# Performance work log

Hardware: AMD Instinct MI355X
Metric: run time of the kernel (lower is better)

## Reference

```python
import jax, jax.numpy as jnp
import numpy as np

T, B, DIN, H, AA, L = 1024, 32, 256, 256, 21, 2


def setup_inputs() -> dict:
    key = jax.random.key(0)
    ks = jax.random.split(key, 8)
    scale = 0.05

    def rn(i, shape):
        return jax.random.normal(ks[i], shape, dtype=jnp.float32) * scale

    return {
        "x": jax.random.normal(ks[0], (B, T, DIN), dtype=jnp.float32),
        "hidden": jnp.zeros((2 * L, B, H), jnp.float32),  # accepted but unused, as in torch forward
        # layer 0: input DIN -> per-direction 4 chunks of H; layer 1: input 2H
        "w_l0": rn(1, (DIN, 2, 4, H)),
        "wc_l0": rn(2, (2, 2, H)),            # [dir, (v_f, v_r), H]
        "b_l0": jnp.zeros((2, 2, H), jnp.float32),  # [dir, (b_f, b_r), H]
        "w_l1": rn(3, (2 * H, 2, 4, H)),
        "wc_l1": rn(4, (2, 2, H)),
        "b_l1": jnp.zeros((2, 2, H), jnp.float32),
        "fc1_w": rn(5, (H, 2 * H)),
        "fc1_b": jnp.zeros((H,), jnp.float32),
        "lp_w": rn(6, (AA, H)),
        "lp_b": jnp.zeros((AA,), jnp.float32),
    }


def _sru_scan(u, vf, vr, bf, br):
    # u: (T, B, 4, H) with chunks [candidate, forget, reset, highway]
    def step(c, ut):
        f = jax.nn.sigmoid(ut[:, 1] + vf * c + bf)
        c2 = f * c + (1.0 - f) * ut[:, 0]
        r = jax.nn.sigmoid(ut[:, 2] + vr * c + br)
        h = r * c2 + (1.0 - r) * ut[:, 3]
        return c2, h

    c0 = jnp.zeros((u.shape[1], u.shape[-1]), u.dtype)
    _, hs = jax.lax.scan(step, c0, u)
    return hs  # (T, B, H)


def _sru_layer(x, w, wc, b):
    # x: (T, B, Din); w: (Din, 2, 4, H)
    U = jnp.einsum('tbd,dnkh->tbnkh', x, w)
    hf = _sru_scan(U[:, :, 0], wc[0, 0], wc[0, 1], b[0, 0], b[0, 1])
    hb = _sru_scan(U[::-1, :, 1], wc[1, 0], wc[1, 1], b[1, 0], b[1, 1])[::-1]
    return jnp.concatenate([hf, hb], axis=-1)  # (T, B, 2H)


def reference(x, hidden, w_l0, wc_l0, b_l0, w_l1, wc_l1, b_l1, fc1_w, fc1_b, lp_w, lp_b):
    h = jnp.transpose(x, (1, 0, 2))  # (T, B, DIN)
    h = _sru_layer(h, w_l0, wc_l0, b_l0)
    h = _sru_layer(h, w_l1, wc_l1, b_l1)
    h = jnp.transpose(h, (1, 0, 2))  # (B, T, 2H)
    h = h @ fc1_w.T + fc1_b
    logits = h @ lp_w.T + lp_b
    return jax.nn.log_softmax(logits, axis=-1)  # (B, T, AA)
```

## Files before the change

### kernel.cpp

```cpp
#include <hip/hip_runtime.h>
#include <hip/hip_bf16.h>

#define T_DIM 1024
#define B_DIM 32
#define DIN_DIM 256
#define H_DIM 256
#define AA_DIM 21
#define M_ROWS (B_DIM * T_DIM)

typedef __attribute__((ext_vector_type(8))) short bf16x8;
typedef __attribute__((ext_vector_type(4))) float f32x4;

typedef __attribute__((address_space(3))) void lds_void;
typedef const __attribute__((address_space(1))) void glb_void;

#define LOG2E_F 1.44269504088896340736f

__device__ __forceinline__ void gload_lds16(const void* g, void* l) {
    __builtin_amdgcn_global_load_lds((glb_void*)g, (lds_void*)l, 16, 0, 0);
}

__device__ __forceinline__ unsigned short f2bu(float f) {
    __hip_bfloat16 h = __float2bfloat16(f);
    unsigned short u;
    __builtin_memcpy(&u, &h, 2);
    return u;
}

#define CVT_V0 2097152
#define CVT_N1 524288
#define CVT_N2 1048576
#define CVT_V3 32768
#define CVT_N4 8192
#define CVT_TOT (CVT_V0 + CVT_N1 + CVT_N2 + CVT_V3 + CVT_N4)
__global__ __launch_bounds__(256) void cvt_all(
    const float* __restrict__ x,  const float* __restrict__ w0,
    const float* __restrict__ w1, const float* __restrict__ fcw,
    const float* __restrict__ lpw,
    __hip_bfloat16* __restrict__ xb,  __hip_bfloat16* __restrict__ w0t,
    __hip_bfloat16* __restrict__ w1t, __hip_bfloat16* __restrict__ fcwb,
    __hip_bfloat16* __restrict__ lpwb)
{
    int i = blockIdx.x * 256 + threadIdx.x;
    if (i < CVT_V0) {
        float4 v = ((const float4*)x)[i];
        ushort4 o = { f2bu(v.x), f2bu(v.y), f2bu(v.z), f2bu(v.w) };
        ((ushort4*)xb)[i] = o;
        return;
    }
    i -= CVT_V0;
    if (i < CVT_N1) {
        int kk = i >> 11, rem = i & 2047;
        int dir = rem >> 10, k = (rem >> 8) & 3, h = rem & 255;
        w0t[(long)(dir * 1024 + h * 4 + k) * 256 + kk] = __float2bfloat16(w0[i]);
        return;
    }
    i -= CVT_N1;
    if (i < CVT_N2) {
        int kk = i >> 11, rem = i & 2047;
        int dir = rem >> 10, k = (rem >> 8) & 3, h = rem & 255;
        w1t[(long)(dir * 1024 + h * 4 + k) * 512 + kk] = __float2bfloat16(w1[i]);
        return;
    }
    i -= CVT_N2;
    if (i < CVT_V3) {
        float4 v = ((const float4*)fcw)[i];
        ushort4 o = { f2bu(v.x), f2bu(v.y), f2bu(v.z), f2bu(v.w) };
        ((ushort4*)fcwb)[i] = o;
        return;
    }
    i -= CVT_V3;
    if (i < CVT_N4) {
        int n = i >> 8, k = i & 255;
        lpwb[i] = __float2bfloat16(n < AA_DIM ? lpw[n * 256 + k] : 0.0f);
    }
}

#define MFMA16(d, a, b) d = __builtin_amdgcn_mfma_f32_16x16x32_bf16(a, b, d, 0, 0, 0)

__device__ __forceinline__ void stage_tile256(
    const __hip_bfloat16* __restrict__ A,
    const __hip_bfloat16* __restrict__ Bt,
    char* buf, long m0, long n0, int K, int kb,
    int wave, int ldrow, int gkoff)
{
#pragma unroll
    for (int i = 0; i < 4; ++i) {
        const int cid = wave * 4 + i;
        const int rc  = cid >> 1;
        const int kh  = cid & 1;
        const long row = rc * 16 + ldrow;
        const int koff = kb + kh * 32 + gkoff;
        gload_lds16(A  + (m0 + row) * (long)K + koff,
                    buf + rc * 2048 + kh * 1024);
        gload_lds16(Bt + (n0 + row) * (long)K + koff,
                    buf + 32768 + rc * 2048 + kh * 1024);
    }
}

__global__ __launch_bounds__(512, 2) void gemm256_u2(
    const __hip_bfloat16* __restrict__ A,
    const __hip_bfloat16* __restrict__ Bt,
    __hip_bfloat16* __restrict__ C,
    int K, int nbShift)
{
    __shared__ __align__(16) char smb[131072];

    const int tid  = threadIdx.x;
    const int lane = tid & 63;
    const int wave = tid >> 6;
    const int wm   = wave >> 2;
    const int wn   = wave & 3;

    const int L  = blockIdx.x;
    const int s  = L >> 3;
    const int nb = s & ((1 << nbShift) - 1);
    const int mb = ((s >> nbShift) << 3) + (L & 7);
    const long n0 = (long)nb * 256;
    const long m0 = (long)mb * 256;

    const int ldrow = lane >> 2;
    const int ldq   = lane & 3;
    const int gq    = ldq ^ ((ldrow >> 1) & 3);
    const int gkoff = gq * 8;

    const int fr = lane & 15;
    const int kq = lane >> 4;
    const int sw = (kq ^ ((fr >> 1) & 3)) * 16;

    f32x4 acc[8][4] = {};
    const int NT = K >> 6;

    stage_tile256(A, Bt, smb,         m0, n0, K, 0,  wave, ldrow, gkoff);
    __builtin_amdgcn_sched_barrier(0);
    stage_tile256(A, Bt, smb + 65536, m0, n0, K, 64, wave, ldrow, gkoff);
    asm volatile("s_waitcnt vmcnt(8)" ::: "memory");
    __builtin_amdgcn_s_barrier();

    for (int kt = 0; kt < NT; ++kt) {
        char* rb = smb + (kt & 1) * 65536;
        const char* Ab = rb + (wm * 8) * 2048;
        const char* Bb = rb + 32768 + (wn * 4) * 2048;
        bf16x8 a0[4], a1[4], bv[4];

#pragma unroll
        for (int i = 0; i < 4; ++i) {
            a0[i] = *(const bf16x8*)(Ab + i * 2048 + fr * 64 + sw);
            bv[i] = *(const bf16x8*)(Bb + i * 2048 + fr * 64 + sw);
        }
        __builtin_amdgcn_s_barrier();
        __builtin_amdgcn_s_setprio(1);
#pragma unroll
        for (int i = 0; i < 4; ++i)
#pragma unroll
            for (int j = 0; j < 4; ++j)
                MFMA16(acc[i][j], a0[i], bv[j]);
        __builtin_amdgcn_s_setprio(0);
        __builtin_amdgcn_s_barrier();

#pragma unroll
        for (int i = 0; i < 4; ++i)
            a1[i] = *(const bf16x8*)(Ab + (4 + i) * 2048 + fr * 64 + sw);
        __builtin_amdgcn_s_barrier();
        __builtin_amdgcn_s_setprio(1);
#pragma unroll
        for (int i = 0; i < 4; ++i)
#pragma unroll
            for (int j = 0; j < 4; ++j)
                MFMA16(acc[4 + i][j], a1[i], bv[j]);
        __builtin_amdgcn_s_setprio(0);
        __builtin_amdgcn_s_barrier();

#pragma unroll
        for (int i = 0; i < 4; ++i) {
            a0[i] = *(const bf16x8*)(Ab + i * 2048 + 1024 + fr * 64 + sw);
            bv[i] = *(const bf16x8*)(Bb + i * 2048 + 1024 + fr * 64 + sw);
        }
        __builtin_amdgcn_s_barrier();
        __builtin_amdgcn_s_setprio(1);
#pragma unroll
        for (int i = 0; i < 4; ++i)
#pragma unroll
            for (int j = 0; j < 4; ++j)
                MFMA16(acc[i][j], a0[i], bv[j]);
        __builtin_amdgcn_s_setprio(0);
        __builtin_amdgcn_s_barrier();

#pragma unroll
        for (int i = 0; i < 4; ++i)
            a1[i] = *(const bf16x8*)(Ab + (4 + i) * 2048 + 1024 + fr * 64 + sw);
        __builtin_amdgcn_s_barrier();
        __builtin_amdgcn_s_setprio(1);
#pragma unroll
        for (int i = 0; i < 4; ++i)
#pragma unroll
            for (int j = 0; j < 4; ++j)
                MFMA16(acc[4 + i][j], a1[i], bv[j]);
        __builtin_amdgcn_s_setprio(0);
        __builtin_amdgcn_s_barrier();

        __builtin_amdgcn_sched_barrier(0);
        if (kt + 2 < NT) {
            stage_tile256(A, Bt, rb, m0, n0, K, (kt + 2) * 64,
                          wave, ldrow, gkoff);
            asm volatile("s_waitcnt vmcnt(8)" ::: "memory");
        } else if (kt + 1 < NT) {
            asm volatile("s_waitcnt vmcnt(0)" ::: "memory");
        }
        __builtin_amdgcn_s_barrier();
    }

    const int col_l = lane & 15;
    const int row_l = (lane >> 4) * 4;
    __hip_bfloat16* smC = (__hip_bfloat16*)smb;
    const int chunk = tid & 31;
    const int rbase = tid >> 5;
#pragma unroll
    for (int p = 0; p < 2; ++p) {
        __syncthreads();
        if (wm == p) {
#pragma unroll
            for (int i = 0; i < 8; ++i)
#pragma unroll
                for (int j = 0; j < 4; ++j)
#pragma unroll
                    for (int r = 0; r < 4; ++r)
                        smC[(i * 16 + row_l + r) * 264 + wn * 64 + j * 16 + col_l] =
                            __float2bfloat16(acc[i][j][r]);
        }
        __syncthreads();
#pragma unroll
        for (int it = 0; it < 8; ++it) {
            const int rr = it * 16 + rbase;
            bf16x8 v = *(const bf16x8*)(smC + rr * 264 + chunk * 8);
            const long gr  = m0 + p * 128 + rr;
            const long gc0 = n0 + chunk * 8;
            const int bI  = (int)(gr >> 10);
            const int t   = (int)(gr & 1023);
            const int dir = (int)(gc0 >> 10);
            const int hg  = ((int)gc0 >> 8) & 3;
            const int beta = bI * 8 + dir * 4 + hg;
            const long base = ((long)beta * 1024 + t) * 256 + ((int)gc0 & 255);
            *(bf16x8*)(C + base) = v;
        }
    }
}

#define SCAN_S 64
#define SCAN_NB (T_DIM / SCAN_S)
#define GRP 16

__device__ __forceinline__ float scan_step(
    uint2 u, float c, float nvf, float nvr, float nbf, float nbr,
    __hip_bfloat16* hq)
{
    float u0, u1, u2, u3;
    unsigned a0 = u.x << 16, a1 = u.x & 0xffff0000u;
    unsigned a2 = u.y << 16, a3 = u.y & 0xffff0000u;
    __builtin_memcpy(&u0, &a0, 4); __builtin_memcpy(&u1, &a1, 4);
    __builtin_memcpy(&u2, &a2, 4); __builtin_memcpy(&u3, &a3, 4);
    const float nf0 = __builtin_fmaf(-LOG2E_F, u1, nbf);
    const float nr0 = __builtin_fmaf(-LOG2E_F, u2, nbr);
    const float ef = __builtin_amdgcn_exp2f(__builtin_fmaf(nvf, c, nf0));
    const float er = __builtin_amdgcn_exp2f(__builtin_fmaf(nvr, c, nr0));
    const float f  = __builtin_amdgcn_rcpf(1.0f + ef);
    const float r  = __builtin_amdgcn_rcpf(1.0f + er);
    const float c2 = __builtin_fmaf(f, c - u0, u0);
    const float hv = __builtin_fmaf(r, c2 - u3, u3);
    *hq = __float2bfloat16(hv);
    return c2;
}

__global__ __launch_bounds__(256) void sru_scan(
    const __hip_bfloat16* __restrict__ U2,
    const float* __restrict__ wc,
    const float* __restrict__ bias,
    __hip_bfloat16* __restrict__ hout)
{
    __shared__ __align__(16) char lds[2 * SCAN_S * 512];
    const int tid  = threadIdx.x;
    const int wave = tid >> 6;
    const int lane = tid & 63;
    const int beta = blockIdx.x;
    const int b    = beta >> 3;
    const int dir  = (beta >> 2) & 1;
    const int hg   = beta & 3;
    const int h    = hg * 64 + lane;

    const char* gslice = (const char*)U2 + (size_t)beta * (1024 * 512);

    const float nvf = -LOG2E_F * wc[(dir * 2 + 0) * H_DIM + h];
    const float nvr = -LOG2E_F * wc[(dir * 2 + 1) * H_DIM + h];
    const float nbf = -LOG2E_F * bias[(dir * 2 + 0) * H_DIM + h];
    const float nbr = -LOG2E_F * bias[(dir * 2 + 1) * H_DIM + h];
    __hip_bfloat16* hp = hout + ((long)(b * 1024 + (dir ? 1023 : 0))) * 512 + dir * 256 + h;
    const long hstep = dir ? -512L : 512L;
    float c = 0.0f;

    const int plane = lane & 31;

    if (wave > 0) {
        for (int p = wave - 1; p < SCAN_S / 2; p += 3) {
            const int sl = 2 * p + (lane >> 5);
            const int t  = dir ? (1023 - sl) : sl;
            gload_lds16(gslice + (size_t)t * 512 + plane * 16, lds + p * 1024);
        }
    }
    __syncthreads();

    for (int bat = 0; bat < SCAN_NB; ++bat) {
        if (wave > 0) {
            if (bat + 1 < SCAN_NB) {
                char* halfN = lds + ((bat + 1) & 1) * (SCAN_S * 512);
                const int tb = (bat + 1) * SCAN_S;
                for (int p = wave - 1; p < SCAN_S / 2; p += 3) {
                    const int sl = tb + 2 * p + (lane >> 5);
                    const int t  = dir ? (1023 - sl) : sl;
                    gload_lds16(gslice + (size_t)t * 512 + plane * 16,
                                halfN + p * 1024);
                }
            }
        } else {
            const char* half = lds + (bat & 1) * (SCAN_S * 512);
            __hip_bfloat16* hq = hp + (long)(bat * SCAN_S) * hstep;
            uint2 qa[GRP], qb[GRP];
#pragma unroll
            for (int j = 0; j < GRP; ++j)
                qa[j] = *(const uint2*)(half + (0 * GRP + j) * 512 + (lane << 3));
#pragma unroll
            for (int j = 0; j < GRP; ++j)
                qb[j] = *(const uint2*)(half + (1 * GRP + j) * 512 + (lane << 3));
#pragma unroll
            for (int j = 0; j < GRP; ++j)
                c = scan_step(qa[j], c, nvf, nvr, nbf, nbr, hq + (long)j * hstep);
#pragma unroll
            for (int j = 0; j < GRP; ++j)
                qa[j] = *(const uint2*)(half + (2 * GRP + j) * 512 + (lane << 3));
#pragma unroll
            for (int j = 0; j < GRP; ++j)
                c = scan_step(qb[j], c, nvf, nvr, nbf, nbr, hq + (long)(GRP + j) * hstep);
#pragma unroll
            for (int j = 0; j < GRP; ++j)
                qb[j] = *(const uint2*)(half + (3 * GRP + j) * 512 + (lane << 3));
#pragma unroll
            for (int j = 0; j < GRP; ++j)
                c = scan_step(qa[j], c, nvf, nvr, nbf, nbr, hq + (long)(2 * GRP + j) * hstep);
#pragma unroll
            for (int j = 0; j < GRP; ++j)
                c = scan_step(qb[j], c, nvf, nvr, nbf, nbr, hq + (long)(3 * GRP + j) * hstep);
        }
        __syncthreads();
    }
}

#define FL_BUF 49152
#define FL_LP  98304
#define FL_SCR 115200
#define FL_TOT 133632

__global__ __launch_bounds__(512, 1) void fc_logits(
    const __hip_bfloat16* __restrict__ A,
    const __hip_bfloat16* __restrict__ Bw,
    const float* __restrict__ fcb,
    const __hip_bfloat16* __restrict__ lpwb,
    const float* __restrict__ lpb,
    float* __restrict__ out)
{
    __shared__ __align__(16) char lds[FL_TOT];
    const int tid  = threadIdx.x;
    const int lane = tid & 63;
    const int wave = tid >> 6;
    const int wm   = wave & 1;
    const int wn   = wave >> 1;
    const long m0  = (long)blockIdx.x * 128;

    const int ldrow = lane >> 2;
    const int ldq   = lane & 3;
    const int gq    = ldq ^ ((ldrow >> 1) & 3);
    const int gkoff = gq * 8;

    const int fr = lane & 15;
    const int kq = lane >> 4;
    const int sw = (kq ^ ((fr >> 1) & 3)) * 16;

    for (int idx = tid; idx < 1024; idx += 512) {
        const int rw = idx >> 5, sl = idx & 31;
        *(bf16x8*)(lds + FL_LP + rw * 528 + sl * 16) =
            *(const bf16x8*)(lpwb + rw * 256 + sl * 8);
    }
    __builtin_amdgcn_sched_barrier(0);

    f32x4 acc[4][4] = {};

#define STAGE_FL(BUF, KB)                                                   \
    do {                                                                    \
        _Pragma("unroll")                                                   \
        for (int i2 = 0; i2 < 6; ++i2) {                                    \
            const int sg = wave * 6 + i2;                        \
            if (sg < 16) {                              \
                const int rc = sg >> 1, kh = sg & 1;                        \
                gload_lds16(A + (m0 + rc * 16 + ldrow) * 512L +             \
                                (KB) + kh * 32 + gkoff,                     \
                            (BUF) + rc * 2048 + kh * 1024);                 \
            } else {                                   \
                const int t2 = sg - 16, rc = t2 >> 1, kh = t2 & 1;          \
                gload_lds16(Bw + (rc * 16 + ldrow) * 512L +                 \
                                 (KB) + kh * 32 + gkoff,                    \
                            (BUF) + 16384 + rc * 2048 + kh * 1024);         \
            }                                                               \
        }                                                                   \
    } while (0)

    STAGE_FL(lds, 0);

    for (int kt = 0; kt < 8; ++kt) {
        char* cur = lds + (kt & 1) * FL_BUF;
        char* nxt = lds + ((kt + 1) & 1) * FL_BUF;
        __builtin_amdgcn_sched_barrier(0);
        if (kt + 1 < 8) {
            STAGE_FL(nxt, (kt + 1) * 64);
            __builtin_amdgcn_sched_barrier(0);
            asm volatile("s_waitcnt vmcnt(6)" ::: "memory");
        } else {
            asm volatile("s_waitcnt vmcnt(0)" ::: "memory");
        }
        __builtin_amdgcn_s_barrier();

#pragma unroll
        for (int ss = 0; ss < 2; ++ss) {
            bf16x8 af[4], bfv[4];
#pragma unroll
            for (int i = 0; i < 4; ++i) {
                af[i]  = *(const bf16x8*)(cur + (wm * 4 + i) * 2048 + ss * 1024 + fr * 64 + sw);
                bfv[i] = *(const bf16x8*)(cur + 16384 + (wn * 4 + i) * 2048 + ss * 1024 + fr * 64 + sw);
            }
            __builtin_amdgcn_s_setprio(1);
#pragma unroll
            for (int i = 0; i < 4; ++i)
#pragma unroll
                for (int j = 0; j < 4; ++j)
                    MFMA16(acc[i][j], af[i], bfv[j]);
            __builtin_amdgcn_s_setprio(0);
        }
        __builtin_amdgcn_s_barrier();
    }
#undef STAGE_FL

    const int col_l = lane & 15;
    const int row_l = (lane >> 4) * 4;
    __hip_bfloat16* fcX = (__hip_bfloat16*)lds;
#pragma unroll
    for (int j = 0; j < 4; ++j) {
        const int gc = wn * 64 + j * 16 + col_l;
        const float bv = fcb[gc];
#pragma unroll
        for (int i = 0; i < 4; ++i)
#pragma unroll
            for (int r = 0; r < 4; ++r)
                fcX[(wm * 64 + i * 16 + row_l + r) * 260 + gc] =
                    __float2bfloat16(acc[i][j][r] + bv);
    }
    __syncthreads();

    const int rb = wave * 16;
    f32x4 acc2[2] = {};
#pragma unroll
    for (int kc = 0; kc < 8; ++kc) {
        bf16x8 afx = *(const bf16x8*)(lds + (rb + fr) * 520 + kc * 64 + kq * 16);
        bf16x8 b0  = *(const bf16x8*)(lds + FL_LP + fr * 528 + kc * 64 + kq * 16);
        bf16x8 b1  = *(const bf16x8*)(lds + FL_LP + (16 + fr) * 528 + kc * 64 + kq * 16);
        MFMA16(acc2[0], afx, b0);
        MFMA16(acc2[1], afx, b1);
    }

    float* smL = (float*)(lds + FL_SCR);
#pragma unroll
    for (int j = 0; j < 2; ++j) {
        const int gc = j * 16 + col_l;
        const float bv = (gc < AA_DIM) ? lpb[gc] : 0.0f;
#pragma unroll
        for (int r = 0; r < 4; ++r)
            smL[(rb + row_l + r) * 36 + gc] = acc2[j][r] + bv;
    }
    __syncthreads();

    if (tid < 128) {
        const float* rowp = smL + tid * 36;
        float m = rowp[0];
#pragma unroll
        for (int a = 1; a < AA_DIM; ++a) m = fmaxf(m, rowp[a]);
        float s = 0.0f;
#pragma unroll
        for (int a = 0; a < AA_DIM; ++a) s += __expf(rowp[a] - m);
        const float lse = __logf(s) + m;
        float* op = out + (m0 + tid) * AA_DIM;
#pragma unroll
        for (int a = 0; a < AA_DIM; ++a) op[a] = rowp[a] - lse;
    }
}

extern "C" void kernel_launch(void* const* d_in, const int* in_sizes, int n_in,
                              void* d_out, int out_size, void* d_ws, size_t ws_size,
                              hipStream_t stream)
{
    const float* x     = (const float*)d_in[0];
    const float* w_l0  = (const float*)d_in[2];
    const float* wc_l0 = (const float*)d_in[3];
    const float* b_l0  = (const float*)d_in[4];
    const float* w_l1  = (const float*)d_in[5];
    const float* wc_l1 = (const float*)d_in[6];
    const float* b_l1  = (const float*)d_in[7];
    const float* fc1_w = (const float*)d_in[8];
    const float* fc1_b = (const float*)d_in[9];
    const float* lp_w  = (const float*)d_in[10];
    const float* lp_b  = (const float*)d_in[11];
    float* out = (float*)d_out;

    char* ws = (char*)d_ws;
    __hip_bfloat16* U      = (__hip_bfloat16*)(ws);
    __hip_bfloat16* h0b    = (__hip_bfloat16*)(ws + 134217728);
    __hip_bfloat16* h1b    = (__hip_bfloat16*)(ws + 167772160);
    __hip_bfloat16* xb     = (__hip_bfloat16*)(ws + 201326592);
    __hip_bfloat16* w0t    = (__hip_bfloat16*)(ws + 218103808);
    __hip_bfloat16* w1t    = (__hip_bfloat16*)(ws + 219152384);
    __hip_bfloat16* fc1wb  = (__hip_bfloat16*)(ws + 221249536);
    __hip_bfloat16* lpwb   = (__hip_bfloat16*)(ws + 221511680);

    cvt_all<<<(CVT_TOT + 255) / 256, 256, 0, stream>>>(
        x, w_l0, w_l1, fc1_w, lp_w, xb, w0t, w1t, fc1wb, lpwb);

    gemm256_u2<<<1024, 512, 0, stream>>>(xb, w0t, U, DIN_DIM, 3);
    sru_scan<<<256, 256, 0, stream>>>(U, wc_l0, b_l0, h0b);
    gemm256_u2<<<1024, 512, 0, stream>>>(h0b, w1t, U, 512, 3);
    sru_scan<<<256, 256, 0, stream>>>(U, wc_l1, b_l1, h1b);

    fc_logits<<<256, 512, 0, stream>>>(h1b, fc1wb, fc1_b, lpwb, lp_b, out);
}
```

Baseline: 378.7 us.

## Load GEMM A operand directly into registers and stage only B through LDS

The GEMM kernel now loads the A tile straight from global memory into per-wave register fragments, double-buffered across k-steps. Only B is staged into LDS, which shrinks shared memory to about 68KB. The wave layout changes from 2x4 to 4x2, so each wave computes 64x128 and reuses each A fragment across 8 B fragments. The aim is to cut LDS traffic and the many per-substep barriers. In exchange, the register budget grows and launch bounds drop to one block per CU, and the A global loads are uncoalesced row reads that depend on L2.

Result: slower. 593.6 us (+56.8%).

```diff
diff --git a/kernel.cpp b/kernel.cpp
--- a/kernel.cpp
+++ b/kernel.cpp
@@ -78,39 +78,19 @@
 
 #define MFMA16(d, a, b) d = __builtin_amdgcn_mfma_f32_16x16x32_bf16(a, b, d, 0, 0, 0)
 
-__device__ __forceinline__ void stage_tile256(
-    const __hip_bfloat16* __restrict__ A,
-    const __hip_bfloat16* __restrict__ Bt,
-    char* buf, long m0, long n0, int K, int kb,
-    int wave, int ldrow, int gkoff)
-{
-#pragma unroll
-    for (int i = 0; i < 4; ++i) {
-        const int cid = wave * 4 + i;
-        const int rc  = cid >> 1;
-        const int kh  = cid & 1;
-        const long row = rc * 16 + ldrow;
-        const int koff = kb + kh * 32 + gkoff;
-        gload_lds16(A  + (m0 + row) * (long)K + koff,
-                    buf + rc * 2048 + kh * 1024);
-        gload_lds16(Bt + (n0 + row) * (long)K + koff,
-                    buf + 32768 + rc * 2048 + kh * 1024);
-    }
-}
-
-__global__ __launch_bounds__(512, 2) void gemm256_u2(
+__global__ __launch_bounds__(512, 1) void gemm256_areg(
     const __hip_bfloat16* __restrict__ A,
     const __hip_bfloat16* __restrict__ Bt,
     __hip_bfloat16* __restrict__ C,
     int K, int nbShift)
 {
-    __shared__ __align__(16) char smb[131072];
+    __shared__ __align__(16) char smb[69632];
 
     const int tid  = threadIdx.x;
     const int lane = tid & 63;
     const int wave = tid >> 6;
-    const int wm   = wave >> 2;
-    const int wn   = wave & 3;
+    const int wm   = wave >> 1;
+    const int wn   = wave & 1;
 
     const int L  = blockIdx.x;
     const int s  = L >> 3;
@@ -128,87 +108,79 @@
     const int kq = lane >> 4;
     const int sw = (kq ^ ((fr >> 1) & 3)) * 16;
 
-    f32x4 acc[8][4] = {};
+    const long arow = m0 + wm * 64 + fr;
+    f32x4 acc[4][8] = {};
+    bf16x8 ar[2][8];
     const int NT = K >> 6;
 
-    stage_tile256(A, Bt, smb,         m0, n0, K, 0,  wave, ldrow, gkoff);
+#define STAGE_B(BUF, KB)                                                    \
+    do {                                                                    \
+        _Pragma("unroll")                                                   \
+        for (int i2 = 0; i2 < 4; ++i2) {                                    \
+            const int cid = wave * 4 + i2;                                  \
+            const int rc  = cid >> 1;                                       \
+            const int kh  = cid & 1;                                        \
+            gload_lds16(Bt + (n0 + rc * 16 + ldrow) * (long)K +             \
+                            (KB) + kh * 32 + gkoff,                         \
+                        (BUF) + rc * 2048 + kh * 1024);                     \
+        }                                                                   \
+    } while (0)
+
+#define LOAD_A(DST, KB)                                                     \
+    do {                                                                    \
+        _Pragma("unroll")                                                   \
+        for (int mf = 0; mf < 4; ++mf)                                      \
+            _Pragma("unroll")                                               \
+            for (int kh = 0; kh < 2; ++kh)                                  \
+                (DST)[mf * 2 + kh] = *(const bf16x8*)(A +                   \
+                    (arow + mf * 16) * (long)K + (KB) + kh * 32 + kq * 8);  \
+    } while (0)
+
+    LOAD_A(ar[0], 0);
+    STAGE_B(smb, 0);
     __builtin_amdgcn_sched_barrier(0);
-    stage_tile256(A, Bt, smb + 65536, m0, n0, K, 64, wave, ldrow, gkoff);
-    asm volatile("s_waitcnt vmcnt(8)" ::: "memory");
+    LOAD_A(ar[1], 64);
+    STAGE_B(smb + 32768, 64);
+    asm volatile("s_waitcnt vmcnt(12)" ::: "memory");
     __builtin_amdgcn_s_barrier();
 
     for (int kt = 0; kt < NT; ++kt) {
-        char* rb = smb + (kt & 1) * 65536;
-        const char* Ab = rb + (wm * 8) * 2048;
-        const char* Bb = rb + 32768 + (wn * 4) * 2048;
-        bf16x8 a0[4], a1[4], bv[4];
-
-#pragma unroll
-        for (int i = 0; i < 4; ++i) {
-            a0[i] = *(const bf16x8*)(Ab + i * 2048 + fr * 64 + sw);
-            bv[i] = *(const bf16x8*)(Bb + i * 2048 + fr * 64 + sw);
-        }
-        __builtin_amdgcn_s_barrier();
+        const char* bb = smb + (kt & 1) * 32768;
+        const int par = kt & 1;
+
         __builtin_amdgcn_s_setprio(1);
 #pragma unroll
-        for (int i = 0; i < 4; ++i)
-#pragma unroll
-            for (int j = 0; j < 4; ++j)
-                MFMA16(acc[i][j], a0[i], bv[j]);
+        for (int kh = 0; kh < 2; ++kh) {
+#pragma unroll
+            for (int nfh = 0; nfh < 2; ++nfh) {
+                bf16x8 bf[4];
+#pragma unroll
+                for (int q = 0; q < 4; ++q)
+                    bf[q] = *(const bf16x8*)(bb + (wn * 8 + nfh * 4 + q) * 2048 +
+                                             kh * 1024 + fr * 64 + sw);
+#pragma unroll
+                for (int mf = 0; mf < 4; ++mf)
+#pragma unroll
+                    for (int q = 0; q < 4; ++q)
+                        MFMA16(acc[mf][nfh * 4 + q], ar[par][mf * 2 + kh], bf[q]);
+            }
+        }
         __builtin_amdgcn_s_setprio(0);
         __builtin_amdgcn_s_barrier();
 
-#pragma unroll
-        for (int i = 0; i < 4; ++i)
-            a1[i] = *(const bf16x8*)(Ab + (4 + i) * 2048 + fr * 64 + sw);
-        __builtin_amdgcn_s_barrier();
-        __builtin_amdgcn_s_setprio(1);
-#pragma unroll
-        for (int i = 0; i < 4; ++i)
-#pragma unroll
-            for (int j = 0; j < 4; ++j)
-                MFMA16(acc[4 + i][j], a1[i], bv[j]);
-        __builtin_amdgcn_s_setprio(0);
-        __builtin_amdgcn_s_barrier();
-
-#pragma unroll
-        for (int i = 0; i < 4; ++i) {
-            a0[i] = *(const bf16x8*)(Ab + i * 2048 + 1024 + fr * 64 + sw);
-            bv[i] = *(const bf16x8*)(Bb + i * 2048 + 1024 + fr * 64 + sw);
-        }
-        __builtin_amdgcn_s_barrier();
-        __builtin_amdgcn_s_setprio(1);
-#pragma unroll
-        for (int i = 0; i < 4; ++i)
-#pragma unroll
-            for (int j = 0; j < 4; ++j)
-                MFMA16(acc[i][j], a0[i], bv[j]);
-        __builtin_amdgcn_s_setprio(0);
-        __builtin_amdgcn_s_barrier();
-
-#pragma unroll
-        for (int i = 0; i < 4; ++i)
-            a1[i] = *(const bf16x8*)(Ab + (4 + i) * 2048 + 1024 + fr * 64 + sw);
-        __builtin_amdgcn_s_barrier();
-        __builtin_amdgcn_s_setprio(1);
-#pragma unroll
-        for (int i = 0; i < 4; ++i)
-#pragma unroll
-            for (int j = 0; j < 4; ++j)
-                MFMA16(acc[4 + i][j], a1[i], bv[j]);
-        __builtin_amdgcn_s_setprio(0);
-        __builtin_amdgcn_s_barrier();
-
         __builtin_amdgcn_sched_barrier(0);
         if (kt + 2 < NT) {
-            stage_tile256(A, Bt, rb, m0, n0, K, (kt + 2) * 64,
-                          wave, ldrow, gkoff);
-            asm volatile("s_waitcnt vmcnt(8)" ::: "memory");
+            LOAD_A(ar[par], (kt + 2) * 64);
+            STAGE_B((char*)bb, (kt + 2) * 64);
+            __builtin_amdgcn_sched_barrier(0);
+            asm volatile("s_waitcnt vmcnt(12)" ::: "memory");
         } else if (kt + 1 < NT) {
             asm volatile("s_waitcnt vmcnt(0)" ::: "memory");
         }
         __builtin_amdgcn_s_barrier();
     }
+#undef STAGE_B
+#undef LOAD_A
 
     const int col_l = lane & 15;
     const int row_l = (lane >> 4) * 4;
@@ -218,15 +190,16 @@
 #pragma unroll
     for (int p = 0; p < 2; ++p) {
         __syncthreads();
-        if (wm == p) {
-#pragma unroll
-            for (int i = 0; i < 8; ++i)
-#pragma unroll
-                for (int j = 0; j < 4; ++j)
+        if ((wm >> 1) == p) {
+#pragma unroll
+            for (int mf = 0; mf < 4; ++mf)
+#pragma unroll
+                for (int nf = 0; nf < 8; ++nf)
 #pragma unroll
                     for (int r = 0; r < 4; ++r)
-                        smC[(i * 16 + row_l + r) * 264 + wn * 64 + j * 16 + col_l] =
-                            __float2bfloat16(acc[i][j][r]);
+                        smC[((wm & 1) * 64 + mf * 16 + row_l + r) * 264 +
+                            wn * 128 + nf * 16 + col_l] =
+                            __float2bfloat16(acc[mf][nf][r]);
         }
         __syncthreads();
 #pragma unroll
@@ -529,9 +502,9 @@
     cvt_all<<<(CVT_TOT + 255) / 256, 256, 0, stream>>>(
         x, w_l0, w_l1, fc1_w, lp_w, xb, w0t, w1t, fc1wb, lpwb);
 
-    gemm256_u2<<<1024, 512, 0, stream>>>(xb, w0t, U, DIN_DIM, 3);
+    gemm256_areg<<<1024, 512, 0, stream>>>(xb, w0t, U, DIN_DIM, 3);
     sru_scan<<<256, 256, 0, stream>>>(U, wc_l0, b_l0, h0b);
-    gemm256_u2<<<1024, 512, 0, stream>>>(h0b, w1t, U, 512, 3);
+    gemm256_areg<<<1024, 512, 0, stream>>>(h0b, w1t, U, 512, 3);
     sru_scan<<<256, 256, 0, stream>>>(U, wc_l1, b_l1, h1b);
 
     fc_logits<<<256, 512, 0, stream>>>(h1b, fc1wb, fc1_b, lpwb, lp_b, out);
```

## Single-buffer fc_logits LDS to fit two blocks per CU

Applied to the files above, without the earlier changes.

Drops the double-buffered LDS staging and the LDS copy of the logits projection weights in fc_logits, cutting shared memory from about 130KB to 65KB and raising launch bounds to two blocks per CU. The second GEMM now reads its weights directly from global memory, and the logit scratch reuses the start of LDS behind an added barrier. The aim is to hide load latency through occupancy rather than in-block prefetch. The cost is that each block now serializes global staging and MFMA work with full syncthreads every k-step.

Result: no change. 383.7 us (+1.3%).

```diff
diff --git a/kernel.cpp b/kernel.cpp
--- a/kernel.cpp
+++ b/kernel.cpp
@@ -353,12 +353,9 @@
     }
 }
 
-#define FL_BUF 49152
-#define FL_LP  98304
-#define FL_SCR 115200
-#define FL_TOT 133632
-
-__global__ __launch_bounds__(512, 1) void fc_logits(
+#define FL2_TOT 66560
+
+__global__ __launch_bounds__(512, 2) void fc_logits(
     const __hip_bfloat16* __restrict__ A,
     const __hip_bfloat16* __restrict__ Bw,
     const float* __restrict__ fcb,
@@ -366,7 +363,7 @@
     const float* __restrict__ lpb,
     float* __restrict__ out)
 {
-    __shared__ __align__(16) char lds[FL_TOT];
+    __shared__ __align__(16) char lds[FL2_TOT];
     const int tid  = threadIdx.x;
     const int lane = tid & 63;
     const int wave = tid >> 6;
@@ -382,13 +379,6 @@
     const int fr = lane & 15;
     const int kq = lane >> 4;
     const int sw = (kq ^ ((fr >> 1) & 3)) * 16;
-
-    for (int idx = tid; idx < 1024; idx += 512) {
-        const int rw = idx >> 5, sl = idx & 31;
-        *(bf16x8*)(lds + FL_LP + rw * 528 + sl * 16) =
-            *(const bf16x8*)(lpwb + rw * 256 + sl * 8);
-    }
-    __builtin_amdgcn_sched_barrier(0);
 
     f32x4 acc[4][4] = {};
 
@@ -411,28 +401,17 @@
         }                                                                   \
     } while (0)
 
-    STAGE_FL(lds, 0);
-
     for (int kt = 0; kt < 8; ++kt) {
-        char* cur = lds + (kt & 1) * FL_BUF;
-        char* nxt = lds + ((kt + 1) & 1) * FL_BUF;
-        __builtin_amdgcn_sched_barrier(0);
-        if (kt + 1 < 8) {
-            STAGE_FL(nxt, (kt + 1) * 64);
-            __builtin_amdgcn_sched_barrier(0);
-            asm volatile("s_waitcnt vmcnt(6)" ::: "memory");
-        } else {
-            asm volatile("s_waitcnt vmcnt(0)" ::: "memory");
-        }
-        __builtin_amdgcn_s_barrier();
+        STAGE_FL(lds, kt * 64);
+        __syncthreads();
 
 #pragma unroll
         for (int ss = 0; ss < 2; ++ss) {
             bf16x8 af[4], bfv[4];
 #pragma unroll
             for (int i = 0; i < 4; ++i) {
-                af[i]  = *(const bf16x8*)(cur + (wm * 4 + i) * 2048 + ss * 1024 + fr * 64 + sw);
-                bfv[i] = *(const bf16x8*)(cur + 16384 + (wn * 4 + i) * 2048 + ss * 1024 + fr * 64 + sw);
+                af[i]  = *(const bf16x8*)(lds + (wm * 4 + i) * 2048 + ss * 1024 + fr * 64 + sw);
+                bfv[i] = *(const bf16x8*)(lds + 16384 + (wn * 4 + i) * 2048 + ss * 1024 + fr * 64 + sw);
             }
             __builtin_amdgcn_s_setprio(1);
 #pragma unroll
@@ -442,7 +421,7 @@
                     MFMA16(acc[i][j], af[i], bfv[j]);
             __builtin_amdgcn_s_setprio(0);
         }
-        __builtin_amdgcn_s_barrier();
+        __syncthreads();
     }
 #undef STAGE_FL
 
@@ -467,13 +446,14 @@
 #pragma unroll
     for (int kc = 0; kc < 8; ++kc) {
         bf16x8 afx = *(const bf16x8*)(lds + (rb + fr) * 520 + kc * 64 + kq * 16);
-        bf16x8 b0  = *(const bf16x8*)(lds + FL_LP + fr * 528 + kc * 64 + kq * 16);
-        bf16x8 b1  = *(const bf16x8*)(lds + FL_LP + (16 + fr) * 528 + kc * 64 + kq * 16);
+        bf16x8 b0  = *(const bf16x8*)(lpwb + fr * 256 + kc * 32 + kq * 8);
+        bf16x8 b1  = *(const bf16x8*)(lpwb + (16 + fr) * 256 + kc * 32 + kq * 8);
         MFMA16(acc2[0], afx, b0);
         MFMA16(acc2[1], afx, b1);
     }
-
-    float* smL = (float*)(lds + FL_SCR);
+    __syncthreads();
+
+    float* smL = (float*)lds;
 #pragma unroll
     for (int j = 0; j < 2; ++j) {
         const int gc = j * 16 + col_l;
```
